# Optimization experiments

Hardware: AMD Instinct MI355X
Metric: run time of the kernel (lower is better)

The kernel has to match this reference:

```python
import jax, jax.numpy as jnp
import numpy as np

EPS = 1e-5

def layer_norm(x, gamma, beta):
    mu = jnp.mean(x, axis=-1, keepdims=True)
    var = jnp.mean(jnp.square(x - mu), axis=-1, keepdims=True)
    return (x - mu) * jax.lax.rsqrt(var + EPS) * gamma + beta

def setup_inputs() -> dict:
    key = jax.random.key(0)
    ks = jax.random.split(key, 12)
    N, E, K = 50000, 100000, 16
    Fn, Fe, H = 128, 128, 128
    node_neighbors = jax.random.randint(ks[0], (N, K), 0, E)      # edges incident to each node
    edge_neighbors = jax.random.randint(ks[1], (E, K), 0, E)      # neighboring edges of each edge
    node_feats = jax.random.normal(ks[2], (N, Fn), dtype=jnp.float32)
    edge_feats = jax.random.normal(ks[3], (E, Fe), dtype=jnp.float32)
    def lin(k, fan_in, fan_out):
        s = 1.0 / np.sqrt(fan_in)
        return jax.random.uniform(k, (fan_in, fan_out), jnp.float32, -s, s)
    W_edge_agg = lin(ks[4], 2 * Fe, H)
    b_edge_agg = jnp.zeros((H,), jnp.float32)
    W_edge_com = lin(ks[5], H, H)
    b_edge_com = jnp.zeros((H,), jnp.float32)
    W_node_agg = lin(ks[6], Fn + H, H)
    b_node_agg = jnp.zeros((H,), jnp.float32)
    W_node_com = lin(ks[7], H, H)
    b_node_com = jnp.zeros((H,), jnp.float32)
    ln_gamma = jnp.ones((H,), jnp.float32)
    ln_beta = jnp.zeros((H,), jnp.float32)
    return dict(node_neighbors=node_neighbors, edge_neighbors=edge_neighbors,
                node_feats=node_feats, edge_feats=edge_feats,
                W_edge_agg=W_edge_agg, b_edge_agg=b_edge_agg,
                W_edge_com=W_edge_com, b_edge_com=b_edge_com,
                W_node_agg=W_node_agg, b_node_agg=b_node_agg,
                W_node_com=W_node_com, b_node_com=b_node_com,
                ln_gamma=ln_gamma, ln_beta=ln_beta)

def reference(node_neighbors, edge_neighbors, node_feats, edge_feats,
              W_edge_agg, b_edge_agg, W_edge_com, b_edge_com,
              W_node_agg, b_node_agg, W_node_com, b_node_com,
              ln_gamma, ln_beta):
    # --- edge path: AGG -> COM -> shared LayerNorm ---
    e_neigh = jnp.take(edge_feats, edge_neighbors, axis=0).mean(axis=1)   # [E,Fe]
    e_agg = jax.nn.relu(jnp.concatenate([edge_feats, e_neigh], axis=-1) @ W_edge_agg + b_edge_agg)
    new_edge_feats = layer_norm(jax.nn.relu(e_agg @ W_edge_com + b_edge_com), ln_gamma, ln_beta)
    # --- node path: gather incident (new) edge feats -> AGG -> COM -> shared LayerNorm ---
    n_neigh = jnp.take(new_edge_feats, node_neighbors, axis=0).mean(axis=1)  # [N,H]
    n_agg = jax.nn.relu(jnp.concatenate([node_feats, n_neigh], axis=-1) @ W_node_agg + b_node_agg)
    new_node_feats = layer_norm(jax.nn.relu(n_agg @ W_node_com + b_node_com), ln_gamma, ln_beta)
    return new_node_feats, new_edge_feats
```

## Files before the change

kernel.cpp:

```cpp
#include <hip/hip_runtime.h>
#include <stdint.h>

typedef short bf16x8 __attribute__((ext_vector_type(8)));
typedef float f32x4 __attribute__((ext_vector_type(4)));

__device__ __forceinline__ unsigned short f2bf(float f) {
    union { float f; unsigned int u; } x; x.f = f;
    unsigned int r = x.u + 0x7FFFu + ((x.u >> 16) & 1u);
    return (unsigned short)(r >> 16);
}

__global__ void prep_weights(const float* __restrict__ w1e, const float* __restrict__ w2e,
                             const float* __restrict__ w1n, const float* __restrict__ w2n,
                             unsigned short* __restrict__ ws) {
    int idx = blockIdx.x * 256 + threadIdx.x;
    if (idx < 32768) {
        int n = idx >> 8, k = idx & 255;
        ws[idx] = f2bf(w1e[k * 128 + n]);
    } else if (idx < 49152) {
        int t = idx - 32768; int n = t >> 7, k = t & 127;
        ws[idx] = f2bf(w2e[k * 128 + n]);
    } else if (idx < 81920) {
        int t = idx - 49152; int n = t >> 8, k = t & 255;
        ws[idx] = f2bf(w1n[k * 128 + n]);
    } else if (idx < 98304) {
        int t = idx - 81920; int n = t >> 7, k = t & 127;
        ws[idx] = f2bf(w2n[k * 128 + n]);
    }
}

__global__ __launch_bounds__(256, 2)
void cagnn_layer(int rows,
                 const float* __restrict__ self_feats,
                 const float* __restrict__ nbr_src,
                 const int*   __restrict__ nbr_idx,
                 const unsigned short* __restrict__ w1t,
                 const unsigned short* __restrict__ w2t,
                 const float* __restrict__ b1,
                 const float* __restrict__ b2,
                 const float* __restrict__ gamma,
                 const float* __restrict__ beta,
                 float* __restrict__ out)
{
    __shared__ __align__(16) char lds[33792 + 16384];
    float* O = (float*)lds;
    char*  Ybase = lds + 33792;

    const int tid  = threadIdx.x;
    const int wid  = tid >> 6;
    const int lane = tid & 63;
    const int base = blockIdx.x * 64;

    {
        const int c0 = 2 * lane;
        for (int rr = wid; rr < 64; rr += 4) {
            const int row = base + rr;
            float sx = 0.f, sy = 0.f, ax = 0.f, ay = 0.f;
            if (row < rows) {
                const float2 v = *(const float2*)(self_feats + (size_t)row * 128 + c0);
                sx = v.x; sy = v.y;
                const int* nb = nbr_idx + (size_t)row * 16;
                #pragma unroll
                for (int k = 0; k < 16; ++k) {
                    const int j = nb[k];
                    const float2 u = *(const float2*)(nbr_src + (size_t)j * 128 + c0);
                    ax += u.x; ay += u.y;
                }
            }
            unsigned int ps = (unsigned int)f2bf(sx) | ((unsigned int)f2bf(sy) << 16);
            unsigned int pa = (unsigned int)f2bf(ax * 0.0625f) | ((unsigned int)f2bf(ay * 0.0625f) << 16);
            const int bs = (rr * 512 + c0 * 2) ^ ((rr & 7) << 4);
            const int bm = (rr * 512 + (128 + c0) * 2) ^ ((rr & 7) << 4);
            *(unsigned int*)(lds + bs) = ps;
            *(unsigned int*)(lds + bm) = pa;
        }
    }

    const int n0 = wid * 32;
    const int bn = lane & 15;
    const int kg = lane >> 4;

    bf16x8 B1[8][2];
    #pragma unroll
    for (int ks = 0; ks < 8; ++ks)
        #pragma unroll
        for (int nt = 0; nt < 2; ++nt)
            B1[ks][nt] = *(const bf16x8*)(w1t + (n0 + nt * 16 + bn) * 256 + ks * 32 + kg * 8);

    __syncthreads();

    f32x4 acc[4][2];
    #pragma unroll
    for (int m = 0; m < 4; ++m)
        #pragma unroll
        for (int nt = 0; nt < 2; ++nt)
            acc[m][nt] = (f32x4){0.f, 0.f, 0.f, 0.f};

    #pragma unroll
    for (int ks = 0; ks < 8; ++ks) {
        bf16x8 a[4];
        #pragma unroll
        for (int m = 0; m < 4; ++m) {
            const int row = m * 16 + bn;
            const int byte = (row * 512 + ks * 64 + kg * 16) ^ ((row & 7) << 4);
            a[m] = *(const bf16x8*)(lds + byte);
        }
        #pragma unroll
        for (int m = 0; m < 4; ++m)
            #pragma unroll
            for (int nt = 0; nt < 2; ++nt)
                acc[m][nt] = __builtin_amdgcn_mfma_f32_16x16x32_bf16(a[m], B1[ks][nt], acc[m][nt], 0, 0, 0);
    }

    float b1v[2] = { b1[n0 + bn], b1[n0 + 16 + bn] };
    #pragma unroll
    for (int m = 0; m < 4; ++m)
        #pragma unroll
        for (int nt = 0; nt < 2; ++nt)
            #pragma unroll
            for (int j = 0; j < 4; ++j) {
                const int row = m * 16 + kg * 4 + j;
                const int col = n0 + nt * 16 + bn;
                float v = fmaxf(acc[m][nt][j] + b1v[nt], 0.f);
                const int byte = (row * 256 + col * 2) ^ ((row & 7) << 4);
                *(unsigned short*)(Ybase + byte) = f2bf(v);
            }

    bf16x8 B2[4][2];
    #pragma unroll
    for (int ks = 0; ks < 4; ++ks)
        #pragma unroll
        for (int nt = 0; nt < 2; ++nt)
            B2[ks][nt] = *(const bf16x8*)(w2t + (n0 + nt * 16 + bn) * 128 + ks * 32 + kg * 8);

    __syncthreads();

    f32x4 acc2[4][2];
    #pragma unroll
    for (int m = 0; m < 4; ++m)
        #pragma unroll
        for (int nt = 0; nt < 2; ++nt)
            acc2[m][nt] = (f32x4){0.f, 0.f, 0.f, 0.f};

    #pragma unroll
    for (int ks = 0; ks < 4; ++ks) {
        bf16x8 a[4];
        #pragma unroll
        for (int m = 0; m < 4; ++m) {
            const int row = m * 16 + bn;
            const int byte = (row * 256 + ks * 64 + kg * 16) ^ ((row & 7) << 4);
            a[m] = *(const bf16x8*)(Ybase + byte);
        }
        #pragma unroll
        for (int m = 0; m < 4; ++m)
            #pragma unroll
            for (int nt = 0; nt < 2; ++nt)
                acc2[m][nt] = __builtin_amdgcn_mfma_f32_16x16x32_bf16(a[m], B2[ks][nt], acc2[m][nt], 0, 0, 0);
    }

    float b2v[2] = { b2[n0 + bn], b2[n0 + 16 + bn] };
    #pragma unroll
    for (int m = 0; m < 4; ++m)
        #pragma unroll
        for (int nt = 0; nt < 2; ++nt)
            #pragma unroll
            for (int j = 0; j < 4; ++j) {
                const int row = m * 16 + kg * 4 + j;
                const int col = n0 + nt * 16 + bn;
                O[row * 132 + col] = fmaxf(acc2[m][nt][j] + b2v[nt], 0.f);
            }

    __syncthreads();

    {
        const int r    = tid >> 2;
        const int part = tid & 3;
        const float* Or = O + r * 132 + part * 32;
        float sum = 0.f, sq = 0.f;
        #pragma unroll
        for (int c = 0; c < 32; c += 4) {
            float4 v = *(const float4*)(Or + c);
            sum += v.x + v.y + v.z + v.w;
            sq  += v.x * v.x + v.y * v.y + v.z * v.z + v.w * v.w;
        }
        sum += __shfl_xor(sum, 1); sq += __shfl_xor(sq, 1);
        sum += __shfl_xor(sum, 2); sq += __shfl_xor(sq, 2);
        const float mean = sum * (1.f / 128.f);
        const float var  = sq * (1.f / 128.f) - mean * mean;
        const float rstd = rsqrtf(var + 1e-5f);
        const int row = base + r;
        if (row < rows) {
            float* op = out + (size_t)row * 128 + part * 32;
            const float* gp = gamma + part * 32;
            const float* bp = beta + part * 32;
            #pragma unroll
            for (int c = 0; c < 32; c += 4) {
                float4 v = *(const float4*)(Or + c);
                float4 g = *(const float4*)(gp + c);
                float4 b = *(const float4*)(bp + c);
                float4 o;
                o.x = (v.x - mean) * rstd * g.x + b.x;
                o.y = (v.y - mean) * rstd * g.y + b.y;
                o.z = (v.z - mean) * rstd * g.z + b.z;
                o.w = (v.w - mean) * rstd * g.w + b.w;
                *(float4*)(op + c) = o;
            }
        }
    }
}

extern "C" void kernel_launch(void* const* d_in, const int* in_sizes, int n_in,
                              void* d_out, int out_size, void* d_ws, size_t ws_size,
                              hipStream_t stream) {
    const int*   node_neighbors = (const int*)d_in[0];
    const int*   edge_neighbors = (const int*)d_in[1];
    const float* node_feats     = (const float*)d_in[2];
    const float* edge_feats     = (const float*)d_in[3];
    const float* W_edge_agg     = (const float*)d_in[4];
    const float* b_edge_agg     = (const float*)d_in[5];
    const float* W_edge_com     = (const float*)d_in[6];
    const float* b_edge_com     = (const float*)d_in[7];
    const float* W_node_agg     = (const float*)d_in[8];
    const float* b_node_agg     = (const float*)d_in[9];
    const float* W_node_com     = (const float*)d_in[10];
    const float* b_node_com     = (const float*)d_in[11];
    const float* ln_gamma       = (const float*)d_in[12];
    const float* ln_beta        = (const float*)d_in[13];

    const int N = in_sizes[2] / 128;
    const int E = in_sizes[3] / 128;

    float* out_nodes = (float*)d_out;
    float* out_edges = (float*)d_out + (size_t)N * 128;

    unsigned short* wsu = (unsigned short*)d_ws;

    prep_weights<<<384, 256, 0, stream>>>(W_edge_agg, W_edge_com, W_node_agg, W_node_com, wsu);

    cagnn_layer<<<(E + 63) / 64, 256, 0, stream>>>(
        E, edge_feats, edge_feats, edge_neighbors,
        wsu + 0, wsu + 32768, b_edge_agg, b_edge_com, ln_gamma, ln_beta, out_edges);

    cagnn_layer<<<(N + 63) / 64, 256, 0, stream>>>(
        N, node_feats, out_edges, node_neighbors,
        wsu + 49152, wsu + 81920, b_node_agg, b_node_com, ln_gamma, ln_beta, out_nodes);
}
```

Baseline: 390.2 us.

## Split neighbor gather-mean into separate kernel and shrink GEMM kernel LDS

```diff
diff --git a/kernel.cpp b/kernel.cpp
--- a/kernel.cpp
+++ b/kernel.cpp
@@ -29,22 +29,51 @@
     }
 }
 
-__global__ __launch_bounds__(256, 2)
-void cagnn_layer(int rows,
-                 const float* __restrict__ self_feats,
-                 const float* __restrict__ nbr_src,
-                 const int*   __restrict__ nbr_idx,
-                 const unsigned short* __restrict__ w1t,
-                 const unsigned short* __restrict__ w2t,
-                 const float* __restrict__ b1,
-                 const float* __restrict__ b2,
-                 const float* __restrict__ gamma,
-                 const float* __restrict__ beta,
-                 float* __restrict__ out)
+__global__ __launch_bounds__(256)
+void gather_mean(int rows,
+                 const float* __restrict__ src,
+                 const int*   __restrict__ idx,
+                 unsigned short* __restrict__ out)
 {
-    __shared__ __align__(16) char lds[33792 + 16384];
+    const int wid  = threadIdx.x >> 6;
+    const int lane = threadIdx.x & 63;
+    const int c0   = 2 * lane;
+    const int step = gridDim.x * 4;
+    for (int row = blockIdx.x * 4 + wid; row < rows; row += step) {
+        const int* nb = idx + (size_t)row * 16;
+        const int4 i0 = *(const int4*)(nb);
+        const int4 i1 = *(const int4*)(nb + 4);
+        const int4 i2 = *(const int4*)(nb + 8);
+        const int4 i3 = *(const int4*)(nb + 12);
+        const int js[16] = { i0.x, i0.y, i0.z, i0.w, i1.x, i1.y, i1.z, i1.w,
+                             i2.x, i2.y, i2.z, i2.w, i3.x, i3.y, i3.z, i3.w };
+        float ax = 0.f, ay = 0.f;
+        #pragma unroll
+        for (int k = 0; k < 16; ++k) {
+            const float2 u = *(const float2*)(src + (size_t)js[k] * 128 + c0);
+            ax += u.x; ay += u.y;
+        }
+        const unsigned int p = (unsigned int)f2bf(ax * 0.0625f)
+                             | ((unsigned int)f2bf(ay * 0.0625f) << 16);
+        *(unsigned int*)(out + (size_t)row * 128 + c0) = p;
+    }
+}
+
+__global__ __launch_bounds__(256, 4)
+void cagnn_gemm(int rows,
+                const float* __restrict__ self_feats,
+                const unsigned short* __restrict__ mean16,
+                const unsigned short* __restrict__ w1t,
+                const unsigned short* __restrict__ w2t,
+                const float* __restrict__ b1,
+                const float* __restrict__ b2,
+                const float* __restrict__ gamma,
+                const float* __restrict__ beta,
+                float* __restrict__ out)
+{
+    __shared__ __align__(16) char lds[33792];
     float* O = (float*)lds;
-    char*  Ybase = lds + 33792;
+    char*  Ybase = lds;
 
     const int tid  = threadIdx.x;
     const int wid  = tid >> 6;
@@ -55,24 +84,18 @@
         const int c0 = 2 * lane;
         for (int rr = wid; rr < 64; rr += 4) {
             const int row = base + rr;
-            float sx = 0.f, sy = 0.f, ax = 0.f, ay = 0.f;
+            float sx = 0.f, sy = 0.f;
+            unsigned int pm = 0;
             if (row < rows) {
                 const float2 v = *(const float2*)(self_feats + (size_t)row * 128 + c0);
                 sx = v.x; sy = v.y;
-                const int* nb = nbr_idx + (size_t)row * 16;
-                #pragma unroll
-                for (int k = 0; k < 16; ++k) {
-                    const int j = nb[k];
-                    const float2 u = *(const float2*)(nbr_src + (size_t)j * 128 + c0);
-                    ax += u.x; ay += u.y;
-                }
-            }
-            unsigned int ps = (unsigned int)f2bf(sx) | ((unsigned int)f2bf(sy) << 16);
-            unsigned int pa = (unsigned int)f2bf(ax * 0.0625f) | ((unsigned int)f2bf(ay * 0.0625f) << 16);
+                pm = *(const unsigned int*)(mean16 + (size_t)row * 128 + c0);
+            }
+            const unsigned int ps = (unsigned int)f2bf(sx) | ((unsigned int)f2bf(sy) << 16);
             const int bs = (rr * 512 + c0 * 2) ^ ((rr & 7) << 4);
             const int bm = (rr * 512 + (128 + c0) * 2) ^ ((rr & 7) << 4);
             *(unsigned int*)(lds + bs) = ps;
-            *(unsigned int*)(lds + bm) = pa;
+            *(unsigned int*)(lds + bm) = pm;
         }
     }
 
@@ -111,6 +134,15 @@
             for (int nt = 0; nt < 2; ++nt)
                 acc[m][nt] = __builtin_amdgcn_mfma_f32_16x16x32_bf16(a[m], B1[ks][nt], acc[m][nt], 0, 0, 0);
     }
+
+    bf16x8 B2[4][2];
+    #pragma unroll
+    for (int ks = 0; ks < 4; ++ks)
+        #pragma unroll
+        for (int nt = 0; nt < 2; ++nt)
+            B2[ks][nt] = *(const bf16x8*)(w2t + (n0 + nt * 16 + bn) * 128 + ks * 32 + kg * 8);
+
+    __syncthreads();
 
     float b1v[2] = { b1[n0 + bn], b1[n0 + 16 + bn] };
     #pragma unroll
@@ -126,13 +158,6 @@
                 *(unsigned short*)(Ybase + byte) = f2bf(v);
             }
 
-    bf16x8 B2[4][2];
-    #pragma unroll
-    for (int ks = 0; ks < 4; ++ks)
-        #pragma unroll
-        for (int nt = 0; nt < 2; ++nt)
-            B2[ks][nt] = *(const bf16x8*)(w2t + (n0 + nt * 16 + bn) * 128 + ks * 32 + kg * 8);
-
     __syncthreads();
 
     f32x4 acc2[4][2];
@@ -157,6 +182,8 @@
             for (int nt = 0; nt < 2; ++nt)
                 acc2[m][nt] = __builtin_amdgcn_mfma_f32_16x16x32_bf16(a[m], B2[ks][nt], acc2[m][nt], 0, 0, 0);
     }
+
+    __syncthreads();
 
     float b2v[2] = { b2[n0 + bn], b2[n0 + 16 + bn] };
     #pragma unroll
@@ -233,15 +260,19 @@
     float* out_nodes = (float*)d_out;
     float* out_edges = (float*)d_out + (size_t)N * 128;
 
-    unsigned short* wsu = (unsigned short*)d_ws;
+    unsigned short* wsu    = (unsigned short*)d_ws;
+    unsigned short* mean_e = wsu + 98304;
+    unsigned short* mean_n = mean_e + (size_t)E * 128;
 
     prep_weights<<<384, 256, 0, stream>>>(W_edge_agg, W_edge_com, W_node_agg, W_node_com, wsu);
 
-    cagnn_layer<<<(E + 63) / 64, 256, 0, stream>>>(
-        E, edge_feats, edge_feats, edge_neighbors,
+    gather_mean<<<2048, 256, 0, stream>>>(E, edge_feats, edge_neighbors, mean_e);
+    cagnn_gemm<<<(E + 63) / 64, 256, 0, stream>>>(
+        E, edge_feats, mean_e,
         wsu + 0, wsu + 32768, b_edge_agg, b_edge_com, ln_gamma, ln_beta, out_edges);
 
-    cagnn_layer<<<(N + 63) / 64, 256, 0, stream>>>(
-        N, node_feats, out_edges, node_neighbors,
+    gather_mean<<<2048, 256, 0, stream>>>(N, out_edges, node_neighbors, mean_n);
+    cagnn_gemm<<<(N + 63) / 64, 256, 0, stream>>>(
+        N, node_feats, mean_n,
         wsu + 49152, wsu + 81920, b_node_agg, b_node_com, ln_gamma, ln_beta, out_nodes);
 }
```

Measured after the change: 426.7 us. 9.4% more time.
